# Performance work log

Measured on AMD Instinct MI355X. Metric: run time of the kernel, lower is better.

The kernel has to match this reference:

```python
import jax, jax.numpy as jnp
import numpy as np

B, S = 512, 256
NUM_LOC, NUM_USERS, D = 50000, 10000, 256
MAX_RECENT = 5
DQ = D // 4            # user/hour/weekday embed dim
TEMP = 3 * DQ          # temporal feature size
H2 = D // 2            # scorer hidden
NEG = -1e9


def setup_inputs() -> dict:
    key = jax.random.key(0)
    ks = jax.random.split(key, 25)
    p = lambda i, shape: jax.random.normal(ks[i], shape, jnp.float32) * 0.02

    locations = jax.random.randint(ks[0], (B, S), 0, NUM_LOC)
    users = jax.random.randint(ks[1], (B, S), 0, NUM_USERS)
    weekdays = jax.random.randint(ks[2], (B, S), 0, 8)
    start_mins = jax.random.randint(ks[3], (B, S), 0, 1440)
    lengths = jax.random.randint(ks[4], (B,), 1, S + 1)  # ragged valid lengths
    mask = jnp.arange(S)[None, :] < lengths[:, None]     # (B,S) bool prefix mask

    return {
        "locations": locations, "users": users, "weekdays": weekdays,
        "start_mins": start_mins, "mask": mask,
        # embedding tables (padding_idx=0 row zeroed, matching torch init)
        "loc_table": p(5, (NUM_LOC, D)).at[0].set(0.0),
        "user_table": p(6, (NUM_USERS, DQ)).at[0].set(0.0),
        "hour_table": p(7, (25, DQ)).at[0].set(0.0),
        "wd_table": p(8, (8, DQ)).at[0].set(0.0),
        # LSTM (PyTorch layout: gates i,f,g,o stacked)
        "W_ih": p(9, (4 * D, D + TEMP)), "W_hh": p(10, (4 * D, D)),
        "b_ih": p(11, (4 * D,)), "b_hh": p(12, (4 * D,)),
        # recent-location scorer MLP
        "sc_W1": p(13, (H2, D + 2)), "sc_b1": p(14, (H2,)),
        "sc_W2": p(15, (1, H2)), "sc_b2": p(16, (1,)),
        # new-location predictor MLP (dropout is identity in eval)
        "np_W1": p(17, (D, D)), "np_b1": p(18, (D,)),
        "np_W2": p(19, (NUM_LOC, D)), "np_b2": p(20, (NUM_LOC,)),
        # mix predictor
        "mx_W": p(21, (1, D)), "mx_b": p(22, (1,)),
    }


def _forward(locations, users, weekdays, start_mins, mask,
             loc_table, user_table, hour_table, wd_table,
             W_ih, W_hh, b_ih, b_hh,
             sc_W1, sc_b1, sc_W2, sc_b2,
             np_W1, np_b1, np_W2, np_b2, mx_W, mx_b):
    gelu = lambda x: jax.nn.gelu(x, approximate=False)  # torch nn.GELU default

    hours = jnp.clip(start_mins // 60, 0, 24)
    temporal = jnp.concatenate(
        [user_table[users], hour_table[hours], wd_table[weekdays]], axis=-1)
    x = jnp.concatenate([loc_table[locations], temporal], axis=-1)  # (B,S,D+TEMP)

    # --- LSTM over time via scan (PyTorch gate order i,f,g,o) ---
    def step(carry, xt):
        h, c = carry
        g = xt @ W_ih.T + b_ih + h @ W_hh.T + b_hh
        i, f, gg, o = jnp.split(g, 4, axis=-1)
        c = jax.nn.sigmoid(f) * c + jax.nn.sigmoid(i) * jnp.tanh(gg)
        h = jax.nn.sigmoid(o) * jnp.tanh(c)
        return (h, c), h

    h0 = jnp.zeros((x.shape[0], D), x.dtype)
    _, outs = jax.lax.scan(step, (h0, h0), jnp.swapaxes(x, 0, 1))
    output = jnp.swapaxes(outs, 0, 1)  # (B,S,D)

    seq_lens = mask.sum(axis=1).astype(jnp.int32) - 1  # last valid index
    bids = jnp.arange(output.shape[0])
    context = output[bids, seq_lens]                   # (B,D)

    # --- vectorized ragged recent-location scoring (j=0 is last visit) ---
    j = jnp.arange(MAX_RECENT)
    idx = seq_lens[:, None] - j[None, :]               # (B,R) indices from end
    valid = idx >= 0                                   # j < seq_len_b
    idxc = jnp.clip(idx, 0, S - 1)
    bidx = bids[:, None]
    rlocs = locations[bidx, idxc]                      # (B,R)
    rtimes = start_mins[bidx, idxc]
    cur_time = start_mins[bids, seq_lens][:, None]
    tdiff = ((cur_time - rtimes).astype(jnp.float32) / 1440.0)[..., None]
    pos = jnp.broadcast_to(j.astype(jnp.float32), rlocs.shape)[..., None]
    feats = jnp.concatenate([loc_table[rlocs], tdiff, pos], axis=-1)  # (B,R,D+2)
    scores = (gelu(feats @ sc_W1.T + sc_b1) @ sc_W2.T + sc_b2)[..., 0]  # (B,R)

    # drop entry jj if some newer valid entry j' < jj has the same location.
    eq = rlocs[:, :, None] == rlocs[:, None, :]        # (B, jj, j')
    newer = (j[:, None] > j[None, :])[None]            # jj > j'
    dup = jnp.any(eq & newer & valid[:, None, :], axis=-1)
    keep = valid & ~dup
    scatter_locs = jnp.where(keep, rlocs, NUM_LOC)     # out-of-range -> dropped

    recent_logits = jnp.full((rlocs.shape[0], NUM_LOC), NEG, jnp.float32)
    recent_logits = recent_logits.at[bidx, scatter_locs].set(scores, mode='drop')

    new_logits = gelu(context @ np_W1.T + np_b1) @ np_W2.T + np_b2  # (B,NUM_LOC)
    mix = jax.nn.sigmoid(context @ mx_W.T + mx_b) * 0.9 + 0.05     # (B,1)
    return mix * recent_logits + (1.0 - mix) * new_logits


def reference(locations, users, weekdays, start_mins, mask,
              loc_table, user_table, hour_table, wd_table,
              W_ih, W_hh, b_ih, b_hh,
              sc_W1, sc_b1, sc_W2, sc_b2,
              np_W1, np_b1, np_W2, np_b2, mx_W, mx_b):
    return _forward(locations, users, weekdays, start_mins, mask,
                    loc_table, user_table, hour_table, wd_table,
                    W_ih, W_hh, b_ih, b_hh,
                    sc_W1, sc_b1, sc_W2, sc_b2,
                    np_W1, np_b1, np_W2, np_b2, mx_W, mx_b)
```

## Files before the change

### kernel.cpp

```cpp
#include <hip/hip_runtime.h>
#include <hip/hip_bf16.h>
#include <math.h>

#define B_ 512
#define S_ 256
#define D_ 256
#define NLOC 50000
#define KX 448
#define G4 1024
#define NEGV -1000000000.0f

typedef __attribute__((ext_vector_type(8))) short short8;
typedef __attribute__((ext_vector_type(4))) float f32x4;

__device__ __forceinline__ float sigmoidf_(float x){ return 1.0f/(1.0f+expf(-x)); }
__device__ __forceinline__ float geluf_(float x){ return 0.5f*x*(1.0f+erff(x*0.70710678118654752f)); }
__device__ __forceinline__ unsigned short f2bf_(float x){
  __hip_bfloat16 h = __float2bfloat16(x);
  return *(unsigned short*)&h;
}
__device__ __forceinline__ float bf2f_(unsigned short u){
  __hip_bfloat16 h = *(__hip_bfloat16*)&u;
  return __bfloat162float(h);
}
__device__ __forceinline__ float fsig_(float x){
  return __fdividef(1.0f, 1.0f + __expf(-x));
}
__device__ __forceinline__ float ftanh_(float x){
  float xc = fminf(fmaxf(x, -15.0f), 15.0f);
  float e = __expf(2.0f*xc);
  return __fdividef(e - 1.0f, e + 1.0f);
}
__device__ __forceinline__ void gld_lds16_(const unsigned short* gsrc, unsigned short* ldst){
  __builtin_amdgcn_global_load_lds((const __attribute__((address_space(1))) void*)gsrc,
                                   (__attribute__((address_space(3))) void*)ldst, 16, 0, 0);
}

__global__ void k_init(int* flag){
  if (blockIdx.x==0 && threadIdx.x==0) *flag = 0;
}

__global__ void k_detect(const unsigned char* m, int* flag){
  int i = blockIdx.x*256 + threadIdx.x;
  if ((i & 1) && i < B_*S_ && m[i]) atomicOr(flag, 1);
}

__global__ void k_seqlen(const void* mp, const int* flag, int* slens){
  int b = blockIdx.x*256 + threadIdx.x;
  if (b >= B_) return;
  int cnt = 0;
  if (*flag){
    const unsigned char* m = (const unsigned char*)mp;
    for (int s=0;s<S_;s++) cnt += (m[b*S_+s] != 0);
  } else {
    const int* m = (const int*)mp;
    for (int s=0;s<S_;s++) cnt += (m[b*S_+s] != 0);
  }
  slens[b] = cnt - 1;
}

__global__ void k_buildw(const float* wih, const float* whh, const float* bih,
                         const float* bhh, unsigned short* Wihbf,
                         unsigned short* Whhbf, float* btot){
  int i = blockIdx.x*256 + threadIdx.x;
  if (i < G4*KX) Wihbf[i] = f2bf_(wih[i]);
  if (i < G4*D_) Whhbf[i] = f2bf_(whh[i]);
  if (i < G4) btot[i] = bih[i] + bhh[i];
}

__global__ __launch_bounds__(256) void k_gx(
    const int* __restrict__ loc, const int* __restrict__ usr,
    const int* __restrict__ wdy, const int* __restrict__ sm,
    const float* __restrict__ loct, const float* __restrict__ usert,
    const float* __restrict__ hourt, const float* __restrict__ wdt,
    const unsigned short* __restrict__ Wihbf, const float* __restrict__ btot,
    unsigned short* __restrict__ Gx){
  __shared__ unsigned short As[128][40];
  int tid = threadIdx.x;
  int n0 = blockIdx.x*128, m0 = blockIdx.y*128;
  int w = tid>>6, lane = tid&63;
  int quad = lane>>4, l16 = lane&15;
  int mw = (w>>1)*64, nw = (w&1)*64;
  f32x4 acc[4][4] = {};
  int r0 = tid>>2, seg = tid&3;
  for (int kt=0; kt<14; kt++){
    int k0 = kt*32;
    int kc = k0 + seg*8;
    #pragma unroll
    for (int rr=0; rr<2; rr++){
      int r = r0 + rr*64;
      int row = m0 + r;
      const float* src;
      if (kc < 256)      src = loct  + (size_t)loc[row]*256 + kc;
      else if (kc < 320) src = usert + (size_t)usr[row]*64 + (kc-256);
      else if (kc < 384) { int s = sm[row]; int hh = s/60; if (hh>24) hh=24; if (hh<0) hh=0;
                           src = hourt + (size_t)hh*64 + (kc-320); }
      else               src = wdt   + (size_t)wdy[row]*64 + (kc-384);
      float4 v0 = *(const float4*)(src);
      float4 v1 = *(const float4*)(src+4);
      short8 pk;
      pk[0]=f2bf_(v0.x); pk[1]=f2bf_(v0.y); pk[2]=f2bf_(v0.z); pk[3]=f2bf_(v0.w);
      pk[4]=f2bf_(v1.x); pk[5]=f2bf_(v1.y); pk[6]=f2bf_(v1.z); pk[7]=f2bf_(v1.w);
      *(short8*)&As[r][seg*8] = pk;
    }
    __syncthreads();
    short8 bfrag[4], afrag[4];
    #pragma unroll
    for (int nt=0; nt<4; nt++)
      bfrag[nt] = *(const short8*)(Wihbf + (size_t)(n0+nw+nt*16+l16)*KX + k0 + quad*8);
    #pragma unroll
    for (int mt=0; mt<4; mt++)
      afrag[mt] = *(const short8*)&As[mw+mt*16+l16][quad*8];
    #pragma unroll
    for (int mt=0; mt<4; mt++)
      #pragma unroll
      for (int nt=0; nt<4; nt++)
        acc[mt][nt] = __builtin_amdgcn_mfma_f32_16x16x32_bf16(afrag[mt], bfrag[nt], acc[mt][nt], 0, 0, 0);
    __syncthreads();
  }
  #pragma unroll
  for (int nt=0; nt<4; nt++){
    int col = n0 + nw + nt*16 + l16;
    float bv = btot[col];
    #pragma unroll
    for (int mt=0; mt<4; mt++){
      #pragma unroll
      for (int i=0; i<4; i++){
        int row = m0 + mw + mt*16 + quad*4 + i;
        int bb = row >> 8, tt = row & 255;
        Gx[((size_t)tt*B_ + bb)*G4 + col] = f2bf_(acc[mt][nt][i] + bv);
      }
    }
  }
}

__global__ __launch_bounds__(512, 2) void k_lstm(
    const unsigned short* __restrict__ Gx,
    const unsigned short* __restrict__ Whhbf,
    float* __restrict__ ctx, const int* __restrict__ slens){
  __shared__ unsigned short h_s[16][264];
  __shared__ unsigned short gx_s[2][16*1024];
  int tid = threadIdx.x;
  int w = tid >> 6, lane = tid & 63;
  int quad = lane >> 4, l16 = lane & 15;
  int b0 = blockIdx.x * 16;
  int dw = w * 32;

  for (int i = tid; i < 16*264; i += 512) ((unsigned short*)h_s)[i] = 0;

  short8 bc[4][2][4];
  #pragma unroll
  for (int q=0;q<4;q++)
    #pragma unroll
    for (int nt=0;nt<2;nt++)
      #pragma unroll
      for (int kt=0;kt<4;kt++)
        bc[q][nt][kt] = *(const short8*)(Whhbf + (size_t)(q*256 + dw + nt*16 + l16)*256 + kt*32 + quad*8);

  float cst[2][4] = {{0.f,0.f,0.f,0.f},{0.f,0.f,0.f,0.f}};
  int slq[4];
  #pragma unroll
  for (int i=0;i<4;i++) slq[i] = slens[b0 + quad*4 + i];

  {
    const unsigned short* src = Gx + (size_t)b0*G4 + w*2048 + lane*8;
    unsigned short* dst = &gx_s[0][w*2048];
    #pragma unroll
    for (int j=0;j<4;j++) gld_lds16_(src + j*512, dst + j*512);
  }
  __syncthreads();

  for (int t=0; t<S_; t++){
    int cur = t & 1;
    int tn = (t < S_-1) ? t+1 : t;
    {
      const unsigned short* src = Gx + ((size_t)tn*B_ + b0)*G4 + w*2048 + lane*8;
      unsigned short* dst = &gx_s[cur^1][w*2048];
      #pragma unroll
      for (int j=0;j<4;j++) gld_lds16_(src + j*512, dst + j*512);
    }

    f32x4 acc[4][2] = {};
    #pragma unroll
    for (int kt=0; kt<8; kt++){
      short8 af = *(const short8*)&h_s[l16][kt*32 + quad*8];
      #pragma unroll
      for (int q=0;q<4;q++)
        #pragma unroll
        for (int nt=0;nt<2;nt++){
          short8 bf;
          if (kt < 4) bf = bc[q][nt][kt];
          else        bf = *(const short8*)(Whhbf + (size_t)(q*256 + dw + nt*16 + l16)*256 + kt*32 + quad*8);
          acc[q][nt] = __builtin_amdgcn_mfma_f32_16x16x32_bf16(af, bf, acc[q][nt], 0, 0, 0);
        }
    }

    asm volatile("s_waitcnt lgkmcnt(0) vmcnt(4)" ::: "memory");
    __builtin_amdgcn_sched_barrier(0);
    __builtin_amdgcn_s_barrier();

    const unsigned int* gxw = (const unsigned int*)&gx_s[cur][0];
    int half = l16 & 1;
    #pragma unroll
    for (int nt=0;nt<2;nt++){
      int d = dw + nt*16 + l16;
      int dbase2 = (dw + nt*16) >> 1;
      #pragma unroll
      for (int i=0;i<4;i++){
        int r = quad*4 + i;
        int base = r*512 + dbase2 + (l16>>1);
        unsigned int u0 = gxw[base];
        unsigned int u1 = gxw[base + 128];
        unsigned int u2 = gxw[base + 256];
        unsigned int u3 = gxw[base + 384];
        unsigned short s0 = half ? (unsigned short)(u0>>16) : (unsigned short)(u0&0xffff);
        unsigned short s1 = half ? (unsigned short)(u1>>16) : (unsigned short)(u1&0xffff);
        unsigned short s2 = half ? (unsigned short)(u2>>16) : (unsigned short)(u2&0xffff);
        unsigned short s3 = half ? (unsigned short)(u3>>16) : (unsigned short)(u3&0xffff);
        float gi = acc[0][nt][i] + bf2f_(s0);
        float gf = acc[1][nt][i] + bf2f_(s1);
        float gg = acc[2][nt][i] + bf2f_(s2);
        float go = acc[3][nt][i] + bf2f_(s3);
        float cn = fsig_(gf)*cst[nt][i] + fsig_(gi)*ftanh_(gg);
        float hn = fsig_(go)*ftanh_(cn);
        cst[nt][i] = cn;
        h_s[r][d] = f2bf_(hn);
        if (t == slq[i]) ctx[(size_t)(b0 + r)*D_ + d] = hn;
      }
    }

    asm volatile("s_waitcnt lgkmcnt(0)" ::: "memory");
    __builtin_amdgcn_sched_barrier(0);
    __builtin_amdgcn_s_barrier();
  }
}

__global__ void k_post1(const float* __restrict__ ctx, const float* __restrict__ W1,
                        const float* __restrict__ b1, const float* __restrict__ mxW,
                        const float* __restrict__ mxb, float* newhid, float* mixv){
  __shared__ float cs[256];
  __shared__ float red[256];
  int b = blockIdx.x, tid = threadIdx.x;
  cs[tid] = ctx[(size_t)b*D_ + tid];
  __syncthreads();
  float a = b1[tid];
  const float* wr = W1 + (size_t)tid*D_;
  for (int k=0; k<D_; k++) a += cs[k]*wr[k];
  newhid[(size_t)b*D_ + tid] = geluf_(a);
  red[tid] = cs[tid]*mxW[tid];
  __syncthreads();
  for (int s=128; s>0; s>>=1){ if (tid<s) red[tid]+=red[tid+s]; __syncthreads(); }
  if (tid==0) mixv[b] = sigmoidf_(red[0]+mxb[0])*0.9f + 0.05f;
}

__global__ void k_recent(const int* __restrict__ loc, const int* __restrict__ sm,
                         const int* __restrict__ slens, const float* __restrict__ loct,
                         const float* __restrict__ W1, const float* __restrict__ b1,
                         const float* __restrict__ W2, const float* __restrict__ b2,
                         float* scores, int* rlocs, int* keep){
  __shared__ int rl[5], vs[5];
  __shared__ float td[5];
  __shared__ float red[128];
  int b = blockIdx.x, tid = threadIdx.x;
  int sl = slens[b];
  if (tid < 5){
    int idx = sl - tid;
    int v = idx >= 0;
    int ic = v ? idx : 0;
    rl[tid] = loc[b*S_ + ic];
    vs[tid] = v;
    int cur = sm[b*S_ + sl];
    td[tid] = (float)(cur - sm[b*S_ + ic]) * (1.0f/1440.0f);
  }
  __syncthreads();
  for (int j=0; j<5; j++){
    const float* lrow = loct + (size_t)rl[j]*D_;
    const float* wr = W1 + (size_t)tid*258;
    float a = b1[tid];
    for (int k=0; k<D_; k++) a += lrow[k]*wr[k];
    a += td[j]*wr[256] + (float)j*wr[257];
    red[tid] = geluf_(a)*W2[tid];
    __syncthreads();
    for (int s=64; s>0; s>>=1){ if (tid<s) red[tid]+=red[tid+s]; __syncthreads(); }
    if (tid==0) scores[b*5+j] = red[0] + b2[0];
    __syncthreads();
  }
  if (tid==0){
    for (int j=0; j<5; j++){
      int dup = 0;
      for (int k=0; k<j; k++) dup |= (rl[j]==rl[k]) && vs[k];
      keep[b*5+j] = vs[j] && !dup;
      rlocs[b*5+j] = rl[j];
    }
  }
}

__global__ __launch_bounds__(256) void k_final(const float* __restrict__ newhid,
    const float* __restrict__ W2, const float* __restrict__ b2,
    const float* __restrict__ mixv, float* __restrict__ out){
  __shared__ float Hs[16][260];
  __shared__ float Wl[64][65];
  int tid = threadIdx.x;
  int l0 = blockIdx.x*64, b0 = blockIdx.y*16;
  int ll = tid & 63, bq = tid >> 6;
  #pragma unroll
  for (int r=0; r<16; r++) Hs[r][tid] = newhid[(size_t)(b0+r)*D_ + tid];
  float acc[4] = {0.f,0.f,0.f,0.f};
  for (int kt=0; kt<4; kt++){
    int k0 = kt*64;
    __syncthreads();
    #pragma unroll
    for (int r=0; r<4; r++){
      int row = 4*r + bq;
      int l = l0 + row;
      Wl[row][ll] = (l < NLOC) ? W2[(size_t)l*D_ + k0 + ll] : 0.f;
    }
    __syncthreads();
    #pragma unroll
    for (int kk=0; kk<64; kk++){
      float wv = Wl[ll][kk];
      #pragma unroll
      for (int bi=0; bi<4; bi++) acc[bi] += wv * Hs[bq*4+bi][k0+kk];
    }
  }
  int l = l0 + ll;
  if (l < NLOC){
    float bias = b2[l];
    #pragma unroll
    for (int bi=0; bi<4; bi++){
      int b = b0 + bq*4 + bi;
      float mx = mixv[b];
      out[(size_t)b*NLOC + l] = mx*NEGV + (1.0f-mx)*(acc[bi] + bias);
    }
  }
}

__global__ void k_scatter(const float* __restrict__ newhid, const float* __restrict__ W2,
                          const float* __restrict__ b2, const float* __restrict__ mixv,
                          const float* __restrict__ scores, const int* __restrict__ rlocs,
                          const int* __restrict__ keep, float* out){
  int b = blockIdx.x, lane = threadIdx.x;
  float mx = mixv[b];
  for (int j=0; j<5; j++){
    if (!keep[b*5+j]) continue;
    int rl = rlocs[b*5+j];
    const float* wr = W2 + (size_t)rl*D_;
    const float* hr = newhid + (size_t)b*D_;
    float a = 0.f;
    #pragma unroll
    for (int q=0; q<4; q++){ int k = lane + 64*q; a += hr[k]*wr[k]; }
    #pragma unroll
    for (int off=32; off>0; off>>=1) a += __shfl_xor(a, off, 64);
    if (lane==0)
      out[(size_t)b*NLOC + rl] = mx*scores[b*5+j] + (1.0f-mx)*(a + b2[rl]);
  }
}

extern "C" void kernel_launch(void* const* d_in, const int* in_sizes, int n_in,
                              void* d_out, int out_size, void* d_ws, size_t ws_size,
                              hipStream_t stream){
  const int* locations   = (const int*)d_in[0];
  const int* users       = (const int*)d_in[1];
  const int* weekdays    = (const int*)d_in[2];
  const int* start_mins  = (const int*)d_in[3];
  const void* mask       = d_in[4];
  const float* loc_table = (const float*)d_in[5];
  const float* user_table= (const float*)d_in[6];
  const float* hour_table= (const float*)d_in[7];
  const float* wd_table  = (const float*)d_in[8];
  const float* W_ih      = (const float*)d_in[9];
  const float* W_hh      = (const float*)d_in[10];
  const float* b_ih      = (const float*)d_in[11];
  const float* b_hh      = (const float*)d_in[12];
  const float* sc_W1     = (const float*)d_in[13];
  const float* sc_b1     = (const float*)d_in[14];
  const float* sc_W2     = (const float*)d_in[15];
  const float* sc_b2     = (const float*)d_in[16];
  const float* np_W1     = (const float*)d_in[17];
  const float* np_b1     = (const float*)d_in[18];
  const float* np_W2     = (const float*)d_in[19];
  const float* np_b2     = (const float*)d_in[20];
  const float* mx_W      = (const float*)d_in[21];
  const float* mx_b      = (const float*)d_in[22];
  float* out = (float*)d_out;

  char* w = (char*)d_ws;
  size_t o = 0;
  auto alloc = [&](size_t bytes)->void*{ void* p = w + o; o += (bytes + 255) & ~(size_t)255; return p; };
  unsigned short* Gx    = (unsigned short*)alloc((size_t)B_*S_*G4*sizeof(short));
  unsigned short* Wihbf = (unsigned short*)alloc((size_t)G4*KX*sizeof(short));
  unsigned short* Whhbf = (unsigned short*)alloc((size_t)G4*D_*sizeof(short));
  float* btot   = (float*)alloc((size_t)G4*sizeof(float));
  float* ctx    = (float*)alloc((size_t)B_*D_*sizeof(float));
  float* newhid = (float*)alloc((size_t)B_*D_*sizeof(float));
  float* mixv   = (float*)alloc((size_t)B_*sizeof(float));
  float* scores = (float*)alloc((size_t)B_*5*sizeof(float));
  int*   slens  = (int*)alloc((size_t)B_*sizeof(int));
  int*   rlocs  = (int*)alloc((size_t)B_*5*sizeof(int));
  int*   keep   = (int*)alloc((size_t)B_*5*sizeof(int));
  int*   flag   = (int*)alloc(sizeof(int));

  k_init<<<1, 64, 0, stream>>>(flag);
  k_detect<<<512, 256, 0, stream>>>((const unsigned char*)mask, flag);
  k_seqlen<<<2, 256, 0, stream>>>(mask, flag, slens);
  k_buildw<<<1792, 256, 0, stream>>>(W_ih, W_hh, b_ih, b_hh, Wihbf, Whhbf, btot);
  k_gx<<<dim3(8,1024), 256, 0, stream>>>(locations, users, weekdays, start_mins,
                                         loc_table, user_table, hour_table, wd_table,
                                         Wihbf, btot, Gx);
  k_lstm<<<32, 512, 0, stream>>>(Gx, Whhbf, ctx, slens);
  k_post1<<<512, 256, 0, stream>>>(ctx, np_W1, np_b1, mx_W, mx_b, newhid, mixv);
  k_recent<<<512, 128, 0, stream>>>(locations, start_mins, slens, loc_table,
                                    sc_W1, sc_b1, sc_W2, sc_b2, scores, rlocs, keep);
  k_final<<<dim3(782,32), 256, 0, stream>>>(newhid, np_W2, np_b2, mixv, out);
  k_scatter<<<512, 64, 0, stream>>>(newhid, np_W2, np_b2, mixv, scores, rlocs, keep, out);
}
```

Before: 3.534 ms.

## Restructure LSTM recurrence weight staging, swizzle hidden-state LDS, and rework tanh

The recurrent LSTM kernel now holds W_hh chunk kt=4 in LDS, loaded once per block, and loads chunks 5-7 from global at the start of each step so those loads overlap the register-resident MFMAs. The hidden-state LDS array drops its padding and uses an XOR swizzle to avoid bank conflicts. The Gx prefetch for the next step moves to after the barrier. tanh switches to a polynomial for small inputs, which trades a little accuracy for fewer near-zero cancellation issues. The changes add LDS use per block (about 64KB more), which may lower occupancy, and the prefetch is less hidden because it now waits for full vmcnt each step.

```diff
diff --git a/kernel.cpp b/kernel.cpp
--- a/kernel.cpp
+++ b/kernel.cpp
@@ -26,10 +26,14 @@
 __device__ __forceinline__ float fsig_(float x){
   return __fdividef(1.0f, 1.0f + __expf(-x));
 }
-__device__ __forceinline__ float ftanh_(float x){
-  float xc = fminf(fmaxf(x, -15.0f), 15.0f);
-  float e = __expf(2.0f*xc);
-  return __fdividef(e - 1.0f, e + 1.0f);
+__device__ __forceinline__ float ftanh2_(float x){
+  float ax = fabsf(x);
+  float x2 = x*x;
+  float tp = x*(1.0f + x2*(-0.3333333333f + x2*(0.1333333333f + x2*(-0.05396825397f))));
+  float e  = __expf(2.0f*fminf(ax, 15.0f));
+  float te = 1.0f - __fdividef(2.0f, e + 1.0f);
+  te = copysignf(te, x);
+  return ax < 0.25f ? tp : te;
 }
 __device__ __forceinline__ void gld_lds16_(const unsigned short* gsrc, unsigned short* ldst){
   __builtin_amdgcn_global_load_lds((const __attribute__((address_space(1))) void*)gsrc,
@@ -138,15 +142,16 @@
     const unsigned short* __restrict__ Gx,
     const unsigned short* __restrict__ Whhbf,
     float* __restrict__ ctx, const int* __restrict__ slens){
-  __shared__ unsigned short h_s[16][264];
+  __shared__ unsigned short h_s[16][256];
   __shared__ unsigned short gx_s[2][16*1024];
+  __shared__ unsigned short whh4[8][8][512];
   int tid = threadIdx.x;
   int w = tid >> 6, lane = tid & 63;
   int quad = lane >> 4, l16 = lane & 15;
   int b0 = blockIdx.x * 16;
   int dw = w * 32;
 
-  for (int i = tid; i < 16*264; i += 512) ((unsigned short*)h_s)[i] = 0;
+  for (int i = tid; i < 16*256; i += 512) ((unsigned short*)h_s)[i] = 0;
 
   short8 bc[4][2][4];
   #pragma unroll
@@ -156,6 +161,13 @@
       #pragma unroll
       for (int kt=0;kt<4;kt++)
         bc[q][nt][kt] = *(const short8*)(Whhbf + (size_t)(q*256 + dw + nt*16 + l16)*256 + kt*32 + quad*8);
+
+  #pragma unroll
+  for (int q=0;q<4;q++)
+    #pragma unroll
+    for (int nt=0;nt<2;nt++)
+      gld_lds16_(Whhbf + (size_t)(q*256 + dw + nt*16 + l16)*256 + 4*32 + quad*8,
+                 &whh4[w][q*2+nt][0]);
 
   float cst[2][4] = {{0.f,0.f,0.f,0.f},{0.f,0.f,0.f,0.f}};
   int slq[4];
@@ -164,40 +176,72 @@
 
   {
     const unsigned short* src = Gx + (size_t)b0*G4 + w*2048 + lane*8;
-    unsigned short* dst = &gx_s[0][w*2048];
-    #pragma unroll
-    for (int j=0;j<4;j++) gld_lds16_(src + j*512, dst + j*512);
-  }
+    #pragma unroll
+    for (int j=0;j<4;j++) gld_lds16_(src + j*512, &gx_s[0][w*2048 + j*512]);
+  }
+  asm volatile("s_waitcnt vmcnt(0) lgkmcnt(0)" ::: "memory");
   __syncthreads();
 
   for (int t=0; t<S_; t++){
     int cur = t & 1;
-    int tn = (t < S_-1) ? t+1 : t;
+    unsigned long long wpa = (unsigned long long)Whhbf;
+    asm volatile("" : "+s"(wpa));
+    const unsigned short* wp = (const unsigned short*)wpa;
+
+    short8 bs[3][8];
+    #pragma unroll
+    for (int s=0;s<2;s++)
+      #pragma unroll
+      for (int q=0;q<4;q++)
+        #pragma unroll
+        for (int nt=0;nt<2;nt++)
+          bs[s][q*2+nt] = *(const short8*)(wp + (size_t)(q*256 + dw + nt*16 + l16)*256 + (5+s)*32 + quad*8);
+
+    f32x4 acc[4][2] = {};
+    #pragma unroll
+    for (int kt=0;kt<4;kt++){
+      short8 a = *(const short8*)((const char*)h_s + l16*512 + ((((kt<<2)|quad) ^ (l16&7))<<4));
+      #pragma unroll
+      for (int q=0;q<4;q++)
+        #pragma unroll
+        for (int nt=0;nt<2;nt++)
+          acc[q][nt] = __builtin_amdgcn_mfma_f32_16x16x32_bf16(a, bc[q][nt][kt], acc[q][nt], 0, 0, 0);
+    }
+    #pragma unroll
+    for (int q=0;q<4;q++)
+      #pragma unroll
+      for (int nt=0;nt<2;nt++)
+        bs[2][q*2+nt] = *(const short8*)(wp + (size_t)(q*256 + dw + nt*16 + l16)*256 + 7*32 + quad*8);
     {
-      const unsigned short* src = Gx + ((size_t)tn*B_ + b0)*G4 + w*2048 + lane*8;
-      unsigned short* dst = &gx_s[cur^1][w*2048];
-      #pragma unroll
-      for (int j=0;j<4;j++) gld_lds16_(src + j*512, dst + j*512);
-    }
-
-    f32x4 acc[4][2] = {};
-    #pragma unroll
-    for (int kt=0; kt<8; kt++){
-      short8 af = *(const short8*)&h_s[l16][kt*32 + quad*8];
+      short8 a = *(const short8*)((const char*)h_s + l16*512 + ((((4<<2)|quad) ^ (l16&7))<<4));
       #pragma unroll
       for (int q=0;q<4;q++)
         #pragma unroll
         for (int nt=0;nt<2;nt++){
-          short8 bf;
-          if (kt < 4) bf = bc[q][nt][kt];
-          else        bf = *(const short8*)(Whhbf + (size_t)(q*256 + dw + nt*16 + l16)*256 + kt*32 + quad*8);
-          acc[q][nt] = __builtin_amdgcn_mfma_f32_16x16x32_bf16(af, bf, acc[q][nt], 0, 0, 0);
+          short8 bf = *(const short8*)&whh4[w][q*2+nt][lane*8];
+          acc[q][nt] = __builtin_amdgcn_mfma_f32_16x16x32_bf16(a, bf, acc[q][nt], 0, 0, 0);
         }
     }
-
-    asm volatile("s_waitcnt lgkmcnt(0) vmcnt(4)" ::: "memory");
+    #pragma unroll
+    for (int s=0;s<3;s++){
+      int kt = 5+s;
+      short8 a = *(const short8*)((const char*)h_s + l16*512 + ((((kt<<2)|quad) ^ (l16&7))<<4));
+      #pragma unroll
+      for (int q=0;q<4;q++)
+        #pragma unroll
+        for (int nt=0;nt<2;nt++)
+          acc[q][nt] = __builtin_amdgcn_mfma_f32_16x16x32_bf16(a, bs[s][q*2+nt], acc[q][nt], 0, 0, 0);
+    }
+
+    asm volatile("s_waitcnt vmcnt(0) lgkmcnt(0)" ::: "memory");
     __builtin_amdgcn_sched_barrier(0);
     __builtin_amdgcn_s_barrier();
+
+    if (t < S_-1){
+      const unsigned short* src = Gx + ((size_t)(t+1)*B_ + b0)*G4 + w*2048 + lane*8;
+      #pragma unroll
+      for (int j=0;j<4;j++) gld_lds16_(src + j*512, &gx_s[cur^1][w*2048 + j*512]);
+    }
 
     const unsigned int* gxw = (const unsigned int*)&gx_s[cur][0];
     int half = l16 & 1;
@@ -205,6 +249,7 @@
     for (int nt=0;nt<2;nt++){
       int d = dw + nt*16 + l16;
       int dbase2 = (dw + nt*16) >> 1;
+      int chunkx = d >> 3;
       #pragma unroll
       for (int i=0;i<4;i++){
         int r = quad*4 + i;
@@ -221,10 +266,10 @@
         float gf = acc[1][nt][i] + bf2f_(s1);
         float gg = acc[2][nt][i] + bf2f_(s2);
         float go = acc[3][nt][i] + bf2f_(s3);
-        float cn = fsig_(gf)*cst[nt][i] + fsig_(gi)*ftanh_(gg);
-        float hn = fsig_(go)*ftanh_(cn);
+        float cn = fsig_(gf)*cst[nt][i] + fsig_(gi)*ftanh2_(gg);
+        float hn = fsig_(go)*ftanh2_(cn);
         cst[nt][i] = cn;
-        h_s[r][d] = f2bf_(hn);
+        *(unsigned short*)((char*)h_s + r*512 + ((chunkx ^ (r&7))<<4) + (d&7)*2) = f2bf_(hn);
         if (t == slq[i]) ctx[(size_t)(b0 + r)*D_ + d] = hn;
       }
     }
```

New measurement: 3.919 ms. +10.9%, slower.
